# Optimization experiments

Measured on AMD Instinct MI355X. Metric: run time of the kernel, lower is better.

The kernel has to match this reference:

```python
import jax, jax.numpy as jnp
import numpy as np

NUM_GRAPHS = 4096
LATENT = 32


def setup_inputs() -> dict:
    key = jax.random.key(0)
    ks = jax.random.split(key, 10)
    N = 2_000_000
    z = jax.random.normal(ks[0], (N, LATENT), dtype=jnp.float32)
    batch = jnp.sort(jax.random.randint(ks[1], (N,), 0, NUM_GRAPHS))
    s = 1.0 / np.sqrt(LATENT)
    att_w1 = jax.random.uniform(ks[2], (LATENT, LATENT), jnp.float32, -s, s)
    att_b1 = jnp.zeros((LATENT,), jnp.float32)
    att_w2 = jax.random.uniform(ks[3], (LATENT, 1), jnp.float32, -s, s)
    att_b2 = jnp.zeros((1,), jnp.float32)
    m1_w = jax.random.uniform(ks[4], (LATENT, 128), jnp.float32, -s, s)
    m1_b = jnp.zeros((128,), jnp.float32)
    s2 = 1.0 / np.sqrt(128)
    m2_w = jax.random.uniform(ks[5], (128, 64), jnp.float32, -s2, s2)
    m2_b = jnp.zeros((64,), jnp.float32)
    s3 = 1.0 / np.sqrt(64)
    m3_w = jax.random.uniform(ks[6], (64, 1), jnp.float32, -s3, s3)
    m3_b = jnp.zeros((1,), jnp.float32)
    return {"z": z, "batch": batch, "att_w1": att_w1, "att_b1": att_b1,
            "att_w2": att_w2, "att_b2": att_b2, "m1_w": m1_w, "m1_b": m1_b,
            "m2_w": m2_w, "m2_b": m2_b, "m3_w": m3_w, "m3_b": m3_b}


def reference(z, batch, att_w1, att_b1, att_w2, att_b2,
              m1_w, m1_b, m2_w, m2_b, m3_w, m3_b):
    # attention scores per node: (N,)
    h = jnp.tanh(z @ att_w1 + att_b1)              # (N, latent)
    alpha = (h @ att_w2 + att_b2)[:, 0]            # (N,)
    alpha = jnp.exp(alpha - jnp.max(alpha))        # global max, as in torch code
    alpha_sum = jax.ops.segment_sum(alpha, batch, num_segments=NUM_GRAPHS)
    alpha = alpha / (alpha_sum[batch] + 1e-8)      # per-graph normalized weights
    graph_z = jax.ops.segment_sum(z * alpha[:, None], batch,
                                  num_segments=NUM_GRAPHS)  # (G, latent)
    # 3-layer MLP (dropout is identity in eval mode)
    x = jax.nn.relu(graph_z @ m1_w + m1_b)
    x = jax.nn.relu(x @ m2_w + m2_b)
    return jax.nn.sigmoid(x @ m3_w + m3_b).reshape(-1)   # (G,)
```

## Files before the change

kernel.cpp:

```cpp
#include <hip/hip_runtime.h>
#include <math.h>

#define N_GRAPHS 4096
#define LATENT 32
#define BLK 256
#define ZSTRIDE 80

typedef short bf16x8 __attribute__((ext_vector_type(8)));
typedef float f32x4  __attribute__((ext_vector_type(4)));
typedef int   i32x4  __attribute__((ext_vector_type(4)));

template<int CTRL>
__device__ __forceinline__ float dpp_shr_add(float x) {
    int y = __builtin_amdgcn_update_dpp(0, __float_as_int(x), CTRL, 0xf, 0xf, false);
    return x + __int_as_float(y);
}

__device__ __forceinline__ float tanh_fast(float x) {
    float e2 = __expf(2.f * x);
    return 1.f - 2.f * __builtin_amdgcn_rcpf(e2 + 1.f);
}

__device__ __forceinline__ unsigned short f32_to_bf16(float f) {
    unsigned int u = __float_as_uint(f);
    u += 0x7fff + ((u >> 16) & 1);
    return (unsigned short)(u >> 16);
}

__global__ __launch_bounds__(256) void zero_ws_kernel(float4* __restrict__ ws) {
    ws[blockIdx.x * 256 + threadIdx.x] = float4{0.f, 0.f, 0.f, 0.f};
}

__global__ __launch_bounds__(BLK, 2) void attn_seg_kernel(
    const float* __restrict__ z, const int* __restrict__ batch,
    const float* __restrict__ w1, const float* __restrict__ b1,
    const float* __restrict__ w2, const float* __restrict__ b2v,
    float* __restrict__ se, float* __restrict__ sez, int n)
{
    __shared__ __align__(16) char smem[26112];
    char*  zb   = smem;
    int*   gls  = (int*)(smem + 20480);
    float* ev   = (float*)(smem + 21504);
    char*  w1T  = smem + 22528;
    float* part = (float*)(smem + 22528);
    float* tab  = (float*)(smem + 25088);

    const int t = threadIdx.x;
    const int lane = t & 63, w = t >> 6;
    const int mrow = lane & 15, grp = lane >> 4;
    const int nd = blockIdx.x * BLK + t;
    const int ndL = (nd < n) ? nd : (n - 1);
    gls[t] = batch[ndL];

    const float b1a = b1[mrow], b1b = b1[mrow + 16];
    const float w2a = w2[mrow], w2b = w2[mrow + 16];

    {
        const size_t blk_f4 = (size_t)blockIdx.x * 2048;
        const size_t max_f4 = (size_t)n * 8;
        const float4* z4 = (const float4*)z;
        float4 v4s[8];
        #pragma unroll
        for (int q = 0; q < 8; ++q) {
            size_t f = blk_f4 + q*256 + t;
            if (f >= max_f4) f = max_f4 - 1;
            v4s[q] = z4[f];
        }
        #pragma unroll
        for (int q = 0; q < 8; ++q) {
            int lo, hi;
            asm("v_cvt_pk_bf16_f32 %0, %1, %2" : "=v"(lo) : "v"(v4s[q].x), "v"(v4s[q].y));
            asm("v_cvt_pk_bf16_f32 %0, %1, %2" : "=v"(hi) : "v"(v4s[q].z), "v"(v4s[q].w));
            const int node = q*32 + (t >> 3), quad = t & 7;
            *(int2*)(zb + node*ZSTRIDE + quad*8) = int2{lo, hi};
        }
    }

    #pragma unroll
    for (int i = 0; i < 4; ++i) {
        int idx = t*4 + i, k = idx >> 5, nc = idx & 31;
        *(unsigned short*)(w1T + nc*ZSTRIDE + k*2) = f32_to_bf16(w1[k*LATENT + nc]);
    }
    __syncthreads();

    bf16x8 A[4];
    #pragma unroll
    for (int T = 0; T < 4; ++T)
        A[T] = *(const bf16x8*)(zb + (w*64 + T*16 + mrow)*ZSTRIDE + grp*16);
    bf16x8 Bh0 = *(const bf16x8*)(w1T + mrow*ZSTRIDE + grp*16);
    bf16x8 Bh1 = *(const bf16x8*)(w1T + (mrow+16)*ZSTRIDE + grp*16);

    const f32x4 c0 = {b1a, b1a, b1a, b1a};
    const f32x4 c1 = {b1b, b1b, b1b, b1b};
    float p[4][4];
    #pragma unroll
    for (int T = 0; T < 4; ++T) {
        f32x4 d0 = __builtin_amdgcn_mfma_f32_16x16x32_bf16(A[T], Bh0, c0, 0, 0, 0);
        f32x4 d1 = __builtin_amdgcn_mfma_f32_16x16x32_bf16(A[T], Bh1, c1, 0, 0, 0);
        #pragma unroll
        for (int r = 0; r < 4; ++r)
            p[T][r] = tanh_fast(d0[r]) * w2a + tanh_fast(d1[r]) * w2b;
    }
    #pragma unroll
    for (int T = 0; T < 4; ++T) {
        #pragma unroll
        for (int r = 0; r < 4; ++r) {
            float v = p[T][r];
            v = dpp_shr_add<0x111>(v);
            v = dpp_shr_add<0x112>(v);
            v = dpp_shr_add<0x114>(v);
            v = dpp_shr_add<0x118>(v);
            p[T][r] = v;
        }
    }
    if (mrow == 15) {
        #pragma unroll
        for (int T = 0; T < 4; ++T)
            *(f32x4*)(tab + w*64 + T*16 + grp*4) = f32x4{p[T][0], p[T][1], p[T][2], p[T][3]};
    }
    __syncthreads();

    float alpha = tab[w*64 + (lane>>4)*16 + ((lane>>2)&3)*4 + (lane&3)] + b2v[0];
    const float e = (nd < n) ? __expf(alpha) : 0.f;
    ev[t] = e;
    __syncthreads();

    {
        const int c  = t >> 4;
        const int kk = t & 15;
        const int base = c * 16;
        const f32x4 e0 = *(const f32x4*)(ev + base);
        const f32x4 e1 = *(const f32x4*)(ev + base + 4);
        const f32x4 e2 = *(const f32x4*)(ev + base + 8);
        const f32x4 e3 = *(const f32x4*)(ev + base + 12);
        const i32x4 g0 = *(const i32x4*)(gls + base);
        const i32x4 g1 = *(const i32x4*)(gls + base + 4);
        const i32x4 g2 = *(const i32x4*)(gls + base + 8);
        const i32x4 g3 = *(const i32x4*)(gls + base + 12);

        float a0 = 0.f, a1 = 0.f;
        int gc = g0[0];
        #pragma unroll
        for (int j = 0; j < 16; ++j) {
            const int   gn = (j < 4) ? g0[j&3] : (j < 8) ? g1[j&3] : (j < 12) ? g2[j&3] : g3[j&3];
            const float ej = (j < 4) ? e0[j&3] : (j < 8) ? e1[j&3] : (j < 12) ? e2[j&3] : e3[j&3];
            const int d = *(const int*)(zb + (base + j)*ZSTRIDE + kk*4);
            if (gn != gc) {
                atomicAdd(&sez[gc*LATENT + 2*kk],     a0);
                atomicAdd(&sez[gc*LATENT + 2*kk + 1], a1);
                a0 = a1 = 0.f; gc = gn;
            }
            a0 = fmaf(ej, __int_as_float((unsigned)d << 16),        a0);
            a1 = fmaf(ej, __int_as_float((unsigned)d & 0xffff0000u), a1);
        }
        *(float2*)(part + c*36 + 2*kk) = float2{a0, a1};

        if (kk == 0) {
            float ae = 0.f;
            int ge = g0[0];
            #pragma unroll
            for (int j = 0; j < 16; ++j) {
                const int   gn = (j < 4) ? g0[j&3] : (j < 8) ? g1[j&3] : (j < 12) ? g2[j&3] : g3[j&3];
                const float ej = (j < 4) ? e0[j&3] : (j < 8) ? e1[j&3] : (j < 12) ? e2[j&3] : e3[j&3];
                if (gn != ge) { atomicAdd(&se[ge], ae); ae = 0.f; ge = gn; }
                ae += ej;
            }
            part[c*36 + 32] = ae;
            ((int*)part)[c*36 + 33] = g3[3];
        }
    }
    __syncthreads();

    if (t < 33) {
        const int col = t;
        float acc = part[col];
        int gc = ((const int*)part)[33];
        #pragma unroll
        for (int cc = 1; cc < 16; ++cc) {
            const int gn = ((const int*)part)[cc*36 + 33];
            if (gn != gc) {
                if (col < 32) atomicAdd(&sez[gc*LATENT + col], acc);
                else          atomicAdd(&se[gc], acc);
                acc = 0.f; gc = gn;
            }
            acc += part[cc*36 + col];
        }
        if (col < 32) atomicAdd(&sez[gc*LATENT + col], acc);
        else          atomicAdd(&se[gc], acc);
    }
}

__global__ __launch_bounds__(64) void mlp_kernel(
    const float* __restrict__ se, const float* __restrict__ sez,
    const float* __restrict__ m1w, const float* __restrict__ m1b,
    const float* __restrict__ m2w, const float* __restrict__ m2b,
    const float* __restrict__ m3w, const float* __restrict__ m3b,
    float* __restrict__ out)
{
    int gidx = blockIdx.x;
    int lane = threadIdx.x;
    float inv = 1.f / (se[gidx] + 1e-8f);
    float gz = (lane < LATENT) ? sez[gidx*LATENT + lane] * inv : 0.f;

    float a0 = m1b[lane], a1 = m1b[lane + 64];
    #pragma unroll
    for (int k = 0; k < LATENT; ++k) {
        float zk = __shfl(gz, k);
        a0 = fmaf(zk, m1w[k*128 + lane], a0);
        a1 = fmaf(zk, m1w[k*128 + lane + 64], a1);
    }
    a0 = fmaxf(a0, 0.f); a1 = fmaxf(a1, 0.f);

    float b = m2b[lane];
    #pragma unroll
    for (int k = 0; k < 64; ++k) {
        float xk = __shfl(a0, k);
        b = fmaf(xk, m2w[k*64 + lane], b);
    }
    #pragma unroll
    for (int k = 0; k < 64; ++k) {
        float xk = __shfl(a1, k);
        b = fmaf(xk, m2w[(k+64)*64 + lane], b);
    }
    b = fmaxf(b, 0.f);

    float p = b * m3w[lane];
    #pragma unroll
    for (int s = 32; s >= 1; s >>= 1)
        p += __shfl_xor(p, s);
    if (lane == 0)
        out[gidx] = 1.f / (1.f + __expf(-(p + m3b[0])));
}

extern "C" void kernel_launch(void* const* d_in, const int* in_sizes, int n_in,
                              void* d_out, int out_size, void* d_ws, size_t ws_size,
                              hipStream_t stream)
{
    const float* z    = (const float*)d_in[0];
    const int*   batch= (const int*)d_in[1];
    const float* aw1  = (const float*)d_in[2];
    const float* ab1  = (const float*)d_in[3];
    const float* aw2  = (const float*)d_in[4];
    const float* ab2  = (const float*)d_in[5];
    const float* m1w  = (const float*)d_in[6];
    const float* m1b  = (const float*)d_in[7];
    const float* m2w  = (const float*)d_in[8];
    const float* m2b  = (const float*)d_in[9];
    const float* m3w  = (const float*)d_in[10];
    const float* m3b  = (const float*)d_in[11];
    float* out = (float*)d_out;

    int n = in_sizes[0] / LATENT;

    float* se  = (float*)d_ws;
    float* sez = se + N_GRAPHS;

    zero_ws_kernel<<<132, 256, 0, stream>>>((float4*)d_ws);

    int blocks = (n + BLK - 1) / BLK;
    attn_seg_kernel<<<blocks, BLK, 0, stream>>>(z, batch, aw1, ab1, aw2, ab2, se, sez, n);
    mlp_kernel<<<N_GRAPHS, 64, 0, stream>>>(se, sez, m1w, m1b, m2w, m2b, m3w, m3b, out);
}
```

Before: 62.25 us.

## Make attention-segment kernel persistent with register prefetch of next tile

```diff
diff --git a/kernel.cpp b/kernel.cpp
--- a/kernel.cpp
+++ b/kernel.cpp
@@ -5,6 +5,7 @@
 #define LATENT 32
 #define BLK 256
 #define ZSTRIDE 80
+#define GRID_ATTN 2048
 
 typedef short bf16x8 __attribute__((ext_vector_type(8)));
 typedef float f32x4  __attribute__((ext_vector_type(4)));
@@ -37,35 +38,50 @@
     const float* __restrict__ w2, const float* __restrict__ b2v,
     float* __restrict__ se, float* __restrict__ sez, int n)
 {
-    __shared__ __align__(16) char smem[26112];
+    __shared__ __align__(16) char smem[28416];
     char*  zb   = smem;
     int*   gls  = (int*)(smem + 20480);
     float* ev   = (float*)(smem + 21504);
     char*  w1T  = smem + 22528;
-    float* part = (float*)(smem + 22528);
-    float* tab  = (float*)(smem + 25088);
+    float* part = (float*)(smem + 25088);
+    float* tab  = (float*)(smem + 27392);
 
     const int t = threadIdx.x;
     const int lane = t & 63, w = t >> 6;
     const int mrow = lane & 15, grp = lane >> 4;
-    const int nd = blockIdx.x * BLK + t;
-    const int ndL = (nd < n) ? nd : (n - 1);
-    gls[t] = batch[ndL];
 
     const float b1a = b1[mrow], b1b = b1[mrow + 16];
     const float w2a = w2[mrow], w2b = w2[mrow + 16];
-
+    const float b2s = b2v[0];
+
+    #pragma unroll
+    for (int i = 0; i < 4; ++i) {
+        int idx = t*4 + i, k = idx >> 5, nc = idx & 31;
+        *(unsigned short*)(w1T + nc*ZSTRIDE + k*2) = f32_to_bf16(w1[k*LATENT + nc]);
+    }
+
+    const int ntiles = (n + BLK - 1) / BLK;
+    const float4* z4 = (const float4*)z;
+    const size_t max_f4 = (size_t)n * 8;
+
+    float4 v4s[8];
+    int    gpref;
     {
         const size_t blk_f4 = (size_t)blockIdx.x * 2048;
-        const size_t max_f4 = (size_t)n * 8;
-        const float4* z4 = (const float4*)z;
-        float4 v4s[8];
         #pragma unroll
         for (int q = 0; q < 8; ++q) {
             size_t f = blk_f4 + q*256 + t;
             if (f >= max_f4) f = max_f4 - 1;
             v4s[q] = z4[f];
         }
+        int nd0 = blockIdx.x * BLK + t;
+        gpref = batch[(nd0 < n) ? nd0 : (n - 1)];
+    }
+
+    for (int tile = blockIdx.x; tile < ntiles; tile += GRID_ATTN) {
+        const int nd = tile * BLK + t;
+
+        gls[t] = gpref;
         #pragma unroll
         for (int q = 0; q < 8; ++q) {
             int lo, hi;
@@ -74,119 +90,125 @@
             const int node = q*32 + (t >> 3), quad = t & 7;
             *(int2*)(zb + node*ZSTRIDE + quad*8) = int2{lo, hi};
         }
-    }
-
-    #pragma unroll
-    for (int i = 0; i < 4; ++i) {
-        int idx = t*4 + i, k = idx >> 5, nc = idx & 31;
-        *(unsigned short*)(w1T + nc*ZSTRIDE + k*2) = f32_to_bf16(w1[k*LATENT + nc]);
-    }
-    __syncthreads();
-
-    bf16x8 A[4];
-    #pragma unroll
-    for (int T = 0; T < 4; ++T)
-        A[T] = *(const bf16x8*)(zb + (w*64 + T*16 + mrow)*ZSTRIDE + grp*16);
-    bf16x8 Bh0 = *(const bf16x8*)(w1T + mrow*ZSTRIDE + grp*16);
-    bf16x8 Bh1 = *(const bf16x8*)(w1T + (mrow+16)*ZSTRIDE + grp*16);
-
-    const f32x4 c0 = {b1a, b1a, b1a, b1a};
-    const f32x4 c1 = {b1b, b1b, b1b, b1b};
-    float p[4][4];
-    #pragma unroll
-    for (int T = 0; T < 4; ++T) {
-        f32x4 d0 = __builtin_amdgcn_mfma_f32_16x16x32_bf16(A[T], Bh0, c0, 0, 0, 0);
-        f32x4 d1 = __builtin_amdgcn_mfma_f32_16x16x32_bf16(A[T], Bh1, c1, 0, 0, 0);
-        #pragma unroll
-        for (int r = 0; r < 4; ++r)
-            p[T][r] = tanh_fast(d0[r]) * w2a + tanh_fast(d1[r]) * w2b;
-    }
-    #pragma unroll
-    for (int T = 0; T < 4; ++T) {
-        #pragma unroll
-        for (int r = 0; r < 4; ++r) {
-            float v = p[T][r];
-            v = dpp_shr_add<0x111>(v);
-            v = dpp_shr_add<0x112>(v);
-            v = dpp_shr_add<0x114>(v);
-            v = dpp_shr_add<0x118>(v);
-            p[T][r] = v;
-        }
-    }
-    if (mrow == 15) {
+        const int nxt = tile + GRID_ATTN;
+        if (nxt < ntiles) {
+            const size_t blk_f4 = (size_t)nxt * 2048;
+            #pragma unroll
+            for (int q = 0; q < 8; ++q) {
+                size_t f = blk_f4 + q*256 + t;
+                if (f >= max_f4) f = max_f4 - 1;
+                v4s[q] = z4[f];
+            }
+            int ndn = nxt * BLK + t;
+            gpref = batch[(ndn < n) ? ndn : (n - 1)];
+        }
+        __syncthreads();
+
+        bf16x8 A[4];
         #pragma unroll
         for (int T = 0; T < 4; ++T)
-            *(f32x4*)(tab + w*64 + T*16 + grp*4) = f32x4{p[T][0], p[T][1], p[T][2], p[T][3]};
-    }
-    __syncthreads();
-
-    float alpha = tab[w*64 + (lane>>4)*16 + ((lane>>2)&3)*4 + (lane&3)] + b2v[0];
-    const float e = (nd < n) ? __expf(alpha) : 0.f;
-    ev[t] = e;
-    __syncthreads();
-
-    {
-        const int c  = t >> 4;
-        const int kk = t & 15;
-        const int base = c * 16;
-        const f32x4 e0 = *(const f32x4*)(ev + base);
-        const f32x4 e1 = *(const f32x4*)(ev + base + 4);
-        const f32x4 e2 = *(const f32x4*)(ev + base + 8);
-        const f32x4 e3 = *(const f32x4*)(ev + base + 12);
-        const i32x4 g0 = *(const i32x4*)(gls + base);
-        const i32x4 g1 = *(const i32x4*)(gls + base + 4);
-        const i32x4 g2 = *(const i32x4*)(gls + base + 8);
-        const i32x4 g3 = *(const i32x4*)(gls + base + 12);
-
-        float a0 = 0.f, a1 = 0.f;
-        int gc = g0[0];
-        #pragma unroll
-        for (int j = 0; j < 16; ++j) {
-            const int   gn = (j < 4) ? g0[j&3] : (j < 8) ? g1[j&3] : (j < 12) ? g2[j&3] : g3[j&3];
-            const float ej = (j < 4) ? e0[j&3] : (j < 8) ? e1[j&3] : (j < 12) ? e2[j&3] : e3[j&3];
-            const int d = *(const int*)(zb + (base + j)*ZSTRIDE + kk*4);
-            if (gn != gc) {
-                atomicAdd(&sez[gc*LATENT + 2*kk],     a0);
-                atomicAdd(&sez[gc*LATENT + 2*kk + 1], a1);
-                a0 = a1 = 0.f; gc = gn;
-            }
-            a0 = fmaf(ej, __int_as_float((unsigned)d << 16),        a0);
-            a1 = fmaf(ej, __int_as_float((unsigned)d & 0xffff0000u), a1);
-        }
-        *(float2*)(part + c*36 + 2*kk) = float2{a0, a1};
-
-        if (kk == 0) {
-            float ae = 0.f;
-            int ge = g0[0];
+            A[T] = *(const bf16x8*)(zb + (w*64 + T*16 + mrow)*ZSTRIDE + grp*16);
+        bf16x8 Bh0 = *(const bf16x8*)(w1T + mrow*ZSTRIDE + grp*16);
+        bf16x8 Bh1 = *(const bf16x8*)(w1T + (mrow+16)*ZSTRIDE + grp*16);
+
+        const f32x4 c0 = {b1a, b1a, b1a, b1a};
+        const f32x4 c1 = {b1b, b1b, b1b, b1b};
+        float p[4][4];
+        #pragma unroll
+        for (int T = 0; T < 4; ++T) {
+            f32x4 d0 = __builtin_amdgcn_mfma_f32_16x16x32_bf16(A[T], Bh0, c0, 0, 0, 0);
+            f32x4 d1 = __builtin_amdgcn_mfma_f32_16x16x32_bf16(A[T], Bh1, c1, 0, 0, 0);
+            #pragma unroll
+            for (int r = 0; r < 4; ++r)
+                p[T][r] = tanh_fast(d0[r]) * w2a + tanh_fast(d1[r]) * w2b;
+        }
+        #pragma unroll
+        for (int T = 0; T < 4; ++T) {
+            #pragma unroll
+            for (int r = 0; r < 4; ++r) {
+                float v = p[T][r];
+                v = dpp_shr_add<0x111>(v);
+                v = dpp_shr_add<0x112>(v);
+                v = dpp_shr_add<0x114>(v);
+                v = dpp_shr_add<0x118>(v);
+                p[T][r] = v;
+            }
+        }
+        if (mrow == 15) {
+            #pragma unroll
+            for (int T = 0; T < 4; ++T)
+                *(f32x4*)(tab + w*64 + T*16 + grp*4) = f32x4{p[T][0], p[T][1], p[T][2], p[T][3]};
+        }
+        __syncthreads();
+
+        float alpha = tab[w*64 + (lane>>4)*16 + ((lane>>2)&3)*4 + (lane&3)] + b2s;
+        const float e = (nd < n) ? __expf(alpha) : 0.f;
+        ev[t] = e;
+        __syncthreads();
+
+        {
+            const int c  = t >> 4;
+            const int kk = t & 15;
+            const int base = c * 16;
+            const f32x4 e0 = *(const f32x4*)(ev + base);
+            const f32x4 e1 = *(const f32x4*)(ev + base + 4);
+            const f32x4 e2 = *(const f32x4*)(ev + base + 8);
+            const f32x4 e3 = *(const f32x4*)(ev + base + 12);
+            const i32x4 g0 = *(const i32x4*)(gls + base);
+            const i32x4 g1 = *(const i32x4*)(gls + base + 4);
+            const i32x4 g2 = *(const i32x4*)(gls + base + 8);
+            const i32x4 g3 = *(const i32x4*)(gls + base + 12);
+
+            float a0 = 0.f, a1 = 0.f;
+            int gc = g0[0];
             #pragma unroll
             for (int j = 0; j < 16; ++j) {
                 const int   gn = (j < 4) ? g0[j&3] : (j < 8) ? g1[j&3] : (j < 12) ? g2[j&3] : g3[j&3];
                 const float ej = (j < 4) ? e0[j&3] : (j < 8) ? e1[j&3] : (j < 12) ? e2[j&3] : e3[j&3];
-                if (gn != ge) { atomicAdd(&se[ge], ae); ae = 0.f; ge = gn; }
-                ae += ej;
-            }
-            part[c*36 + 32] = ae;
-            ((int*)part)[c*36 + 33] = g3[3];
-        }
-    }
-    __syncthreads();
-
-    if (t < 33) {
-        const int col = t;
-        float acc = part[col];
-        int gc = ((const int*)part)[33];
-        #pragma unroll
-        for (int cc = 1; cc < 16; ++cc) {
-            const int gn = ((const int*)part)[cc*36 + 33];
-            if (gn != gc) {
-                if (col < 32) atomicAdd(&sez[gc*LATENT + col], acc);
-                else          atomicAdd(&se[gc], acc);
-                acc = 0.f; gc = gn;
-            }
-            acc += part[cc*36 + col];
-        }
-        if (col < 32) atomicAdd(&sez[gc*LATENT + col], acc);
-        else          atomicAdd(&se[gc], acc);
+                const int d = *(const int*)(zb + (base + j)*ZSTRIDE + kk*4);
+                if (gn != gc) {
+                    atomicAdd(&sez[gc*LATENT + 2*kk],     a0);
+                    atomicAdd(&sez[gc*LATENT + 2*kk + 1], a1);
+                    a0 = a1 = 0.f; gc = gn;
+                }
+                a0 = fmaf(ej, __int_as_float((unsigned)d << 16),        a0);
+                a1 = fmaf(ej, __int_as_float((unsigned)d & 0xffff0000u), a1);
+            }
+            *(float2*)(part + c*36 + 2*kk) = float2{a0, a1};
+
+            if (kk == 0) {
+                float ae = 0.f;
+                int ge = g0[0];
+                #pragma unroll
+                for (int j = 0; j < 16; ++j) {
+                    const int   gn = (j < 4) ? g0[j&3] : (j < 8) ? g1[j&3] : (j < 12) ? g2[j&3] : g3[j&3];
+                    const float ej = (j < 4) ? e0[j&3] : (j < 8) ? e1[j&3] : (j < 12) ? e2[j&3] : e3[j&3];
+                    if (gn != ge) { atomicAdd(&se[ge], ae); ae = 0.f; ge = gn; }
+                    ae += ej;
+                }
+                part[c*36 + 32] = ae;
+                ((int*)part)[c*36 + 33] = g3[3];
+            }
+        }
+        __syncthreads();
+
+        if (t < 33) {
+            const int col = t;
+            float acc = part[col];
+            int gc = ((const int*)part)[33];
+            #pragma unroll
+            for (int cc = 1; cc < 16; ++cc) {
+                const int gn = ((const int*)part)[cc*36 + 33];
+                if (gn != gc) {
+                    if (col < 32) atomicAdd(&sez[gc*LATENT + col], acc);
+                    else          atomicAdd(&se[gc], acc);
+                    acc = 0.f; gc = gn;
+                }
+                acc += part[cc*36 + col];
+            }
+            if (col < 32) atomicAdd(&sez[gc*LATENT + col], acc);
+            else          atomicAdd(&se[gc], acc);
+        }
     }
 }
 
@@ -257,7 +279,6 @@
 
     zero_ws_kernel<<<132, 256, 0, stream>>>((float4*)d_ws);
 
-    int blocks = (n + BLK - 1) / BLK;
-    attn_seg_kernel<<<blocks, BLK, 0, stream>>>(z, batch, aw1, ab1, aw2, ab2, se, sez, n);
+    attn_seg_kernel<<<GRID_ATTN, BLK, 0, stream>>>(z, batch, aw1, ab1, aw2, ab2, se, sez, n);
     mlp_kernel<<<N_GRAPHS, 64, 0, stream>>>(se, sez, m1w, m1b, m2w, m2b, m3w, m3b, out);
 }
```

After: 73.04 us. 1.17x slower.
